# Optimization experiments

Hardware: AMD Instinct MI355X
Metric: run time of the kernel (lower is better)

Reference implementation:

```python
import jax, jax.numpy as jnp
import numpy as np

B = 1024          # batch of subject-object pairs
D_IN_HALF = 2048  # sbj/obj feature width; cat -> input_len = 4096
D_OUT = 1024      # output_len (embedding / label-vec width)
N_LABELS = 128    # number of relation labels in codebook


def setup_inputs() -> dict:
    key = jax.random.key(0)
    ks = jax.random.split(key, 7)
    s = 0.02  # small init scale for weights
    return {
        "sbj_vec": jax.random.normal(ks[0], (B, D_IN_HALF), jnp.float32),
        "obj_vec": jax.random.normal(ks[1], (B, D_IN_HALF), jnp.float32),
        "W1": jax.random.normal(ks[2], (2 * D_IN_HALF, D_OUT), jnp.float32) * s,
        "b1": jax.random.normal(ks[3], (D_OUT,), jnp.float32) * s,
        "W2": jax.random.normal(ks[4], (D_OUT, D_OUT), jnp.float32) * s,
        "b2": jax.random.normal(ks[5], (D_OUT,), jnp.float32) * s,
        "label_vecs": jax.random.normal(ks[6], (N_LABELS, D_OUT), jnp.float32),
    }


def reference(sbj_vec, obj_vec, W1, b1, W2, b2, label_vecs):
    # Sequential(ReLU, Dropout(eval=identity), Linear) applied twice.
    x = jnp.concatenate([sbj_vec, obj_vec], axis=1)          # [B, 2*D_IN_HALF]
    hidden = jax.nn.relu(x) @ W1 + b1                        # [B, D_OUT]
    emb = jax.nn.relu(hidden) @ W2 + b2                      # [B, D_OUT]
    # order_sim vs every label vector, fully batched (replaces per-sample loop):
    # sim[b, l] = -|| relu(label_vecs[l] - emb[b]) ||_2
    diff = jax.nn.relu(label_vecs[None, :, :] - emb[:, None, :])  # [B, L, D_OUT]
    scores = -jnp.sqrt(jnp.sum(diff * diff, axis=2))              # [B, L]
    return scores
```

## Files before the change

### kernel.cpp

```cpp
#include <hip/hip_runtime.h>
#include <math.h>

constexpr int Bn = 1024, DH = 2048, K1 = 4096, DO = 1024, NL = 128;
constexpr int MN = Bn * DO;

typedef __bf16 bf16x8 __attribute__((ext_vector_type(8)));
typedef short  s16x8  __attribute__((ext_vector_type(8)));
typedef float  f32x4  __attribute__((ext_vector_type(4)));

__device__ __forceinline__ unsigned short f2bf(float f) {
  union { float f; unsigned u; } v; v.f = f;
  unsigned r = v.u + 0x7FFFu + ((v.u >> 16) & 1u);
  return (unsigned short)(r >> 16);
}
__device__ __forceinline__ float bf2f(unsigned h) {
  union { unsigned u; float f; } v; v.u = h << 16; return v.f;
}

__global__ __launch_bounds__(256)
void prep(const float* __restrict__ sbj, const float* __restrict__ obj,
          const float* __restrict__ W1, const float* __restrict__ W2,
          unsigned short* __restrict__ Abf,
          unsigned short* __restrict__ W1t, unsigned short* __restrict__ W2t) {
  const int tid = threadIdx.x;
  if (blockIdx.x < 2048) {
    const int t = blockIdx.x * 256 + tid;
    const int m = t >> 9;
    const int k = (t & 511) << 3;
    const float* src = (k < DH) ? sbj + (size_t)m * DH + k
                                : obj + (size_t)m * DH + (k - DH);
    const float4 a = ((const float4*)src)[0];
    const float4 b = ((const float4*)src)[1];
    uint4 o;
    o.x = (unsigned)f2bf(fmaxf(a.x, 0.f)) | ((unsigned)f2bf(fmaxf(a.y, 0.f)) << 16);
    o.y = (unsigned)f2bf(fmaxf(a.z, 0.f)) | ((unsigned)f2bf(fmaxf(a.w, 0.f)) << 16);
    o.z = (unsigned)f2bf(fmaxf(b.x, 0.f)) | ((unsigned)f2bf(fmaxf(b.y, 0.f)) << 16);
    o.w = (unsigned)f2bf(fmaxf(b.z, 0.f)) | ((unsigned)f2bf(fmaxf(b.w, 0.f)) << 16);
    *(uint4*)&Abf[(size_t)m * K1 + k] = o;
    return;
  }
  __shared__ float tl[64][65];
  const int tb = blockIdx.x - 2048;
  int by = tb >> 4;
  const int c0 = (tb & 15) * 64;
  const float* in; unsigned short* out; int R;
  if (by < 64) { in = W1; out = W1t; R = K1; }
  else         { in = W2; out = W2t; R = DO; by -= 64; }
  const int r0 = by * 64;
  {
    const int rr = tid >> 4, cc = (tid & 15) * 4;
    #pragma unroll
    for (int i = 0; i < 4; ++i) {
      const float4 v = *(const float4*)&in[(size_t)(r0 + rr + i * 16) * DO + c0 + cc];
      tl[rr + i * 16][cc + 0] = v.x; tl[rr + i * 16][cc + 1] = v.y;
      tl[rr + i * 16][cc + 2] = v.z; tl[rr + i * 16][cc + 3] = v.w;
    }
  }
  __syncthreads();
  {
    const int r4 = (tid & 15) * 4;
    #pragma unroll
    for (int i = 0; i < 4; ++i) {
      const int cr = i * 16 + (tid >> 4);
      uint2 o;
      o.x = (unsigned)f2bf(tl[r4 + 0][cr]) | ((unsigned)f2bf(tl[r4 + 1][cr]) << 16);
      o.y = (unsigned)f2bf(tl[r4 + 2][cr]) | ((unsigned)f2bf(tl[r4 + 3][cr]) << 16);
      *(uint2*)&out[(size_t)(c0 + cr) * R + r0 + r4] = o;
    }
  }
}

template <int KSLICE>
__global__ __launch_bounds__(256, 2)
void mfma_gemm(const unsigned short* __restrict__ A,
               const unsigned short* __restrict__ Bt,
               unsigned short* __restrict__ P, int K) {
  __shared__ __align__(16) unsigned short smem[2][2 * 128 * 64];

  const int tid = threadIdx.x;
  const int w = tid >> 6, l = tid & 63;
  const int bid = blockIdx.x;
  const int z = bid & 7, t = bid >> 3;
  const int m0 = (t >> 3) * 128, n0 = (t & 7) * 128;
  const int kb = z * KSLICE;

  f32x4 acc[4][4] = {};

  constexpr int NIT = KSLICE / 64;

  auto stage = [&](int buf, int it) {
    const int k0 = kb + it * 64;
    unsigned short* LA = smem[buf];
    unsigned short* LB = smem[buf] + 128 * 64;
    #pragma unroll
    for (int i = 0; i < 4; ++i) {
      const int c = i * 256 + tid, row = c >> 3, kc = c & 7;
      const int kcg = kc ^ (row & 7);
      __builtin_amdgcn_global_load_lds(
          (const __attribute__((address_space(1))) unsigned int*)(A + (size_t)(m0 + row) * K + k0 + kcg * 8),
          (__attribute__((address_space(3))) unsigned int*)&LA[c * 8], 16, 0, 0);
    }
    #pragma unroll
    for (int i = 0; i < 4; ++i) {
      const int c = i * 256 + tid, row = c >> 3, kc = c & 7;
      const int kcg = kc ^ (row & 7);
      __builtin_amdgcn_global_load_lds(
          (const __attribute__((address_space(1))) unsigned int*)(Bt + (size_t)(n0 + row) * K + k0 + kcg * 8),
          (__attribute__((address_space(3))) unsigned int*)&LB[c * 8], 16, 0, 0);
    }
  };

  stage(0, 0);
  int cur = 0;
  for (int it = 0; it < NIT; ++it) {
    __syncthreads();
    if (it + 1 < NIT) stage(cur ^ 1, it + 1);

    const unsigned short* LA = smem[cur];
    const unsigned short* LB = smem[cur] + 128 * 64;
    #pragma unroll
    for (int s = 0; s < 2; ++s) {
      const int kcq = s * 4 + (l >> 4);
      bf16x8 af[4], bfr[4];
      #pragma unroll
      for (int i = 0; i < 4; ++i) {
        const int r = (w >> 1) * 64 + i * 16 + (l & 15);
        const int kca = kcq ^ (r & 7);
        af[i] = __builtin_bit_cast(bf16x8, *(const s16x8*)&LA[(r * 8 + kca) * 8]);
      }
      #pragma unroll
      for (int j = 0; j < 4; ++j) {
        const int rr = (w & 1) * 64 + j * 16 + (l & 15);
        const int kcb = kcq ^ (rr & 7);
        bfr[j] = __builtin_bit_cast(bf16x8, *(const s16x8*)&LB[(rr * 8 + kcb) * 8]);
      }
      #pragma unroll
      for (int i = 0; i < 4; ++i)
        #pragma unroll
        for (int j = 0; j < 4; ++j)
          acc[i][j] = __builtin_amdgcn_mfma_f32_16x16x32_bf16(af[i], bfr[j], acc[i][j], 0, 0, 0);
    }
    cur ^= 1;
  }

  unsigned short* Pz = P + (size_t)z * MN;
  #pragma unroll
  for (int i = 0; i < 4; ++i) {
    #pragma unroll
    for (int r = 0; r < 4; ++r) {
      const int m = m0 + (w >> 1) * 64 + i * 16 + (l >> 4) * 4 + r;
      #pragma unroll
      for (int j = 0; j < 4; ++j) {
        const int n = n0 + (w & 1) * 64 + j * 16 + (l & 15);
        Pz[(size_t)m * DO + n] = f2bf(acc[i][j][r]);
      }
    }
  }
}

__global__ __launch_bounds__(256)
void combine1(const unsigned short* __restrict__ P, const float* __restrict__ bias,
              unsigned short* __restrict__ out) {
  const int row = blockIdx.x, t = threadIdx.x;
  const size_t base = (size_t)row * DO + t * 4;
  float s0 = 0.f, s1 = 0.f, s2 = 0.f, s3 = 0.f;
  #pragma unroll
  for (int c = 0; c < 8; ++c) {
    const uint2 wv = *(const uint2*)&P[(size_t)c * MN + base];
    s0 += bf2f(wv.x & 0xFFFFu); s1 += bf2f(wv.x >> 16);
    s2 += bf2f(wv.y & 0xFFFFu); s3 += bf2f(wv.y >> 16);
  }
  const f32x4 bb = *(const f32x4*)&bias[t * 4];
  s0 = fmaxf(s0 + bb[0], 0.f); s1 = fmaxf(s1 + bb[1], 0.f);
  s2 = fmaxf(s2 + bb[2], 0.f); s3 = fmaxf(s3 + bb[3], 0.f);
  uint2 o;
  o.x = (unsigned)f2bf(s0) | ((unsigned)f2bf(s1) << 16);
  o.y = (unsigned)f2bf(s2) | ((unsigned)f2bf(s3) << 16);
  *(uint2*)&out[base] = o;
}

__global__ __launch_bounds__(256, 2)
void gemm2_full(const unsigned short* __restrict__ A,
                const unsigned short* __restrict__ Bt,
                const float* __restrict__ b2, float* __restrict__ E) {
  __shared__ __align__(16) unsigned short smem[2][2 * 64 * 128];

  const int tid = threadIdx.x;
  const int w = tid >> 6, l = tid & 63;
  const int bid = blockIdx.x;
  const int m0 = (bid >> 4) * 64, n0 = (bid & 15) * 64;

  f32x4 acc[4][4] = {};

  auto stage = [&](int buf, int it) {
    const int k0 = it * 128;
    unsigned short* LA = smem[buf];
    unsigned short* LB = smem[buf] + 64 * 128;
    #pragma unroll
    for (int i = 0; i < 4; ++i) {
      const int c = i * 256 + tid, m = c >> 4, kc = c & 15;
      const int kcg = (kc & 8) | ((kc & 7) ^ (m & 7));
      __builtin_amdgcn_global_load_lds(
          (const __attribute__((address_space(1))) unsigned int*)(A + (size_t)(m0 + m) * DO + k0 + kcg * 8),
          (__attribute__((address_space(3))) unsigned int*)&LA[c * 8], 16, 0, 0);
    }
    #pragma unroll
    for (int i = 0; i < 4; ++i) {
      const int c = i * 256 + tid, n = c >> 4, kc = c & 15;
      const int kcg = (kc & 8) | ((kc & 7) ^ (n & 7));
      __builtin_amdgcn_global_load_lds(
          (const __attribute__((address_space(1))) unsigned int*)(Bt + (size_t)(n0 + n) * DO + k0 + kcg * 8),
          (__attribute__((address_space(3))) unsigned int*)&LB[c * 8], 16, 0, 0);
    }
  };

  stage(0, 0);
  int cur = 0;
  for (int it = 0; it < 8; ++it) {
    __syncthreads();
    if (it + 1 < 8) stage(cur ^ 1, it + 1);

    const unsigned short* LA = smem[cur];
    const unsigned short* LB = smem[cur] + 64 * 128;
    const int kcq = w * 4 + (l >> 4);
    bf16x8 af[4], bfr[4];
    #pragma unroll
    for (int i = 0; i < 4; ++i) {
      const int r = i * 16 + (l & 15);
      const int kca = (kcq & 8) | ((kcq & 7) ^ (r & 7));
      af[i]  = __builtin_bit_cast(bf16x8, *(const s16x8*)&LA[(r * 16 + kca) * 8]);
      bfr[i] = __builtin_bit_cast(bf16x8, *(const s16x8*)&LB[(r * 16 + kca) * 8]);
    }
    #pragma unroll
    for (int i = 0; i < 4; ++i)
      #pragma unroll
      for (int j = 0; j < 4; ++j)
        acc[i][j] = __builtin_amdgcn_mfma_f32_16x16x32_bf16(af[i], bfr[j], acc[i][j], 0, 0, 0);
    cur ^= 1;
  }
  __syncthreads();

  float* red = (float*)smem;
  if (w >= 2) {
    #pragma unroll
    for (int i = 0; i < 4; ++i)
      #pragma unroll
      for (int j = 0; j < 4; ++j)
        *(f32x4*)&red[(w - 2) * 4096 + ((i * 4 + j) * 64 + l) * 4] = acc[i][j];
  }
  __syncthreads();
  if (w < 2) {
    #pragma unroll
    for (int i = 0; i < 4; ++i)
      #pragma unroll
      for (int j = 0; j < 4; ++j)
        acc[i][j] += *(const f32x4*)&red[w * 4096 + ((i * 4 + j) * 64 + l) * 4];
  }
  __syncthreads();
  if (w == 1) {
    #pragma unroll
    for (int i = 0; i < 2; ++i)
      #pragma unroll
      for (int j = 0; j < 4; ++j)
        *(f32x4*)&red[((i * 4 + j) * 64 + l) * 4] = acc[i][j];
  } else if (w == 0) {
    #pragma unroll
    for (int i = 0; i < 2; ++i)
      #pragma unroll
      for (int j = 0; j < 4; ++j)
        *(f32x4*)&red[2048 + ((i * 4 + j) * 64 + l) * 4] = acc[i + 2][j];
  }
  __syncthreads();
  if (w >= 2) return;

  if (w == 0) {
    #pragma unroll
    for (int i = 0; i < 2; ++i) {
      #pragma unroll
      for (int j = 0; j < 4; ++j)
        acc[i][j] += *(const f32x4*)&red[((i * 4 + j) * 64 + l) * 4];
      #pragma unroll
      for (int r = 0; r < 4; ++r) {
        const int m = m0 + i * 16 + (l >> 4) * 4 + r;
        #pragma unroll
        for (int j = 0; j < 4; ++j) {
          const int n = n0 + j * 16 + (l & 15);
          E[(size_t)m * DO + n] = acc[i][j][r] + b2[n];
        }
      }
    }
  } else {
    #pragma unroll
    for (int i = 0; i < 2; ++i) {
      #pragma unroll
      for (int j = 0; j < 4; ++j)
        acc[i + 2][j] += *(const f32x4*)&red[2048 + ((i * 4 + j) * 64 + l) * 4];
      #pragma unroll
      for (int r = 0; r < 4; ++r) {
        const int m = m0 + (i + 2) * 16 + (l >> 4) * 4 + r;
        #pragma unroll
        for (int j = 0; j < 4; ++j) {
          const int n = n0 + j * 16 + (l & 15);
          E[(size_t)m * DO + n] = acc[i + 2][j][r] + b2[n];
        }
      }
    }
  }
}

__global__ __launch_bounds__(256)
void score_partial(const float* __restrict__ E, const float* __restrict__ labels,
                   float* __restrict__ SP) {
  __shared__ float es[64][33];
  __shared__ float ls[64][132];
  const int tid = threadIdx.x;
  const int b0 = blockIdx.x * 32;

  const int tb = tid & 15;
  const int tl = tid >> 4;
  float acc[2][8] = {};

  #pragma unroll
  for (int ch = 0; ch < 2; ++ch) {
    const int d0 = blockIdx.y * 128 + ch * 64;
    if (ch) __syncthreads();

    #pragma unroll
    for (int i = 0; i < 2; ++i) {
      const int fi = tid + i * 256;
      const int b = fi >> 4, dq = fi & 15;
      const float4 v = *(const float4*)&E[(size_t)(b0 + b) * DO + d0 + dq * 4];
      es[dq * 4 + 0][b] = v.x; es[dq * 4 + 1][b] = v.y;
      es[dq * 4 + 2][b] = v.z; es[dq * 4 + 3][b] = v.w;
    }
    #pragma unroll
    for (int i = 0; i < 8; ++i) {
      const int fi = tid + i * 256;
      const int lr = fi >> 4, dq = fi & 15;
      const float4 v = *(const float4*)&labels[(size_t)lr * DO + d0 + dq * 4];
      ls[dq * 4 + 0][lr] = v.x; ls[dq * 4 + 1][lr] = v.y;
      ls[dq * 4 + 2][lr] = v.z; ls[dq * 4 + 3][lr] = v.w;
    }
    __syncthreads();

    for (int dd = 0; dd < 64; ++dd) {
      const float e0 = es[dd][tb * 2 + 0];
      const float e1 = es[dd][tb * 2 + 1];
      const float4 l0 = *(const float4*)&ls[dd][tl * 8];
      const float4 l1 = *(const float4*)&ls[dd][tl * 8 + 4];
      const float lv[8] = {l0.x, l0.y, l0.z, l0.w, l1.x, l1.y, l1.z, l1.w};
      #pragma unroll
      for (int j = 0; j < 8; ++j) {
        float t0 = fmaxf(lv[j] - e0, 0.f); acc[0][j] = fmaf(t0, t0, acc[0][j]);
        float t1 = fmaxf(lv[j] - e1, 0.f); acc[1][j] = fmaf(t1, t1, acc[1][j]);
      }
    }
  }

  float* SPz = SP + (size_t)blockIdx.y * (Bn * NL);
  #pragma unroll
  for (int i = 0; i < 2; ++i) {
    const size_t base = (size_t)(b0 + tb * 2 + i) * NL + tl * 8;
    float4 v0 = {acc[i][0], acc[i][1], acc[i][2], acc[i][3]};
    float4 v1 = {acc[i][4], acc[i][5], acc[i][6], acc[i][7]};
    *(float4*)&SPz[base]     = v0;
    *(float4*)&SPz[base + 4] = v1;
  }
}

__global__ __launch_bounds__(256)
void score_reduce(const float* __restrict__ SP, float* __restrict__ out) {
  const size_t i4 = (size_t)blockIdx.x * 256 + threadIdx.x;
  f32x4 s = ((const f32x4*)SP)[i4];
  #pragma unroll
  for (int c = 1; c < 8; ++c) s += ((const f32x4*)SP)[(size_t)c * 32768 + i4];
  f32x4 o = {-sqrtf(s[0]), -sqrtf(s[1]), -sqrtf(s[2]), -sqrtf(s[3])};
  ((f32x4*)out)[i4] = o;
}

extern "C" void kernel_launch(void* const* d_in, const int* in_sizes, int n_in,
                              void* d_out, int out_size, void* d_ws, size_t ws_size,
                              hipStream_t stream) {
  const float* sbj  = (const float*)d_in[0];
  const float* obj  = (const float*)d_in[1];
  const float* W1   = (const float*)d_in[2];
  const float* b1   = (const float*)d_in[3];
  const float* W2   = (const float*)d_in[4];
  const float* b2   = (const float*)d_in[5];
  const float* labs = (const float*)d_in[6];
  float* scores = (float*)d_out;
  char* ws = (char*)d_ws;

  unsigned short* Abf = (unsigned short*)(ws);
  unsigned short* W1t = (unsigned short*)(ws + (8ull << 20));
  unsigned short* W2t = (unsigned short*)(ws + (16ull << 20));
  unsigned short* H   = (unsigned short*)(ws + (18ull << 20));
  float* E  = (float*)(ws + (20ull << 20));
  unsigned short* P = (unsigned short*)(ws + (24ull << 20));
  float* SP = (float*)(ws + (40ull << 20));

  dim3 blk(256);
  prep<<<dim3(2048 + 1280), blk, 0, stream>>>(sbj, obj, W1, W2, Abf, W1t, W2t);

  mfma_gemm<512><<<dim3(512), blk, 0, stream>>>(Abf, W1t, P, K1);
  combine1<<<dim3(Bn), blk, 0, stream>>>(P, b1, H);
  gemm2_full<<<dim3(256), blk, 0, stream>>>(H, W2t, b2, E);
  score_partial<<<dim3(32, 8), blk, 0, stream>>>(E, labs, SP);
  score_reduce<<<dim3(128), blk, 0, stream>>>(SP, scores);
}
```

Before: 133.6 us.

## Fuse activation ReLU and bf16 conversion into GEMM1 A-tile loading

Removes the prep pass that wrote a bf16 copy of the concatenated ReLU'd activations. GEMM1 now loads fp32 sbj/obj tiles into registers, applies ReLU, converts to bf16 and writes them to swizzled LDS, with the global load overlapped with the MFMA loop. This saves a full write and re-read of the 8 MB bf16 activation buffer, at the cost of more register pressure and ALU work inside the GEMM. combine1 is also widened to 8 elements per thread with half as many blocks.

Result: no change. 136.2 us (+2.0%).

```diff
diff --git a/kernel.cpp b/kernel.cpp
--- a/kernel.cpp
+++ b/kernel.cpp
@@ -18,29 +18,11 @@
 }
 
 __global__ __launch_bounds__(256)
-void prep(const float* __restrict__ sbj, const float* __restrict__ obj,
-          const float* __restrict__ W1, const float* __restrict__ W2,
-          unsigned short* __restrict__ Abf,
+void prep(const float* __restrict__ W1, const float* __restrict__ W2,
           unsigned short* __restrict__ W1t, unsigned short* __restrict__ W2t) {
   const int tid = threadIdx.x;
-  if (blockIdx.x < 2048) {
-    const int t = blockIdx.x * 256 + tid;
-    const int m = t >> 9;
-    const int k = (t & 511) << 3;
-    const float* src = (k < DH) ? sbj + (size_t)m * DH + k
-                                : obj + (size_t)m * DH + (k - DH);
-    const float4 a = ((const float4*)src)[0];
-    const float4 b = ((const float4*)src)[1];
-    uint4 o;
-    o.x = (unsigned)f2bf(fmaxf(a.x, 0.f)) | ((unsigned)f2bf(fmaxf(a.y, 0.f)) << 16);
-    o.y = (unsigned)f2bf(fmaxf(a.z, 0.f)) | ((unsigned)f2bf(fmaxf(a.w, 0.f)) << 16);
-    o.z = (unsigned)f2bf(fmaxf(b.x, 0.f)) | ((unsigned)f2bf(fmaxf(b.y, 0.f)) << 16);
-    o.w = (unsigned)f2bf(fmaxf(b.z, 0.f)) | ((unsigned)f2bf(fmaxf(b.w, 0.f)) << 16);
-    *(uint4*)&Abf[(size_t)m * K1 + k] = o;
-    return;
-  }
   __shared__ float tl[64][65];
-  const int tb = blockIdx.x - 2048;
+  const int tb = blockIdx.x;
   int by = tb >> 4;
   const int c0 = (tb & 15) * 64;
   const float* in; unsigned short* out; int R;
@@ -72,9 +54,9 @@
 
 template <int KSLICE>
 __global__ __launch_bounds__(256, 2)
-void mfma_gemm(const unsigned short* __restrict__ A,
+void mfma_gemm(const float* __restrict__ sbj, const float* __restrict__ obj,
                const unsigned short* __restrict__ Bt,
-               unsigned short* __restrict__ P, int K) {
+               unsigned short* __restrict__ P) {
   __shared__ __align__(16) unsigned short smem[2][2 * 128 * 64];
 
   const int tid = threadIdx.x;
@@ -84,37 +66,62 @@
   const int m0 = (t >> 3) * 128, n0 = (t & 7) * 128;
   const int kb = z * KSLICE;
 
+  const float* __restrict__ Asrc = (z < 4) ? sbj : obj;
+  const int cb = kb - ((z < 4) ? 0 : DH);
+
   f32x4 acc[4][4] = {};
+  float4 areg[4][2];
 
   constexpr int NIT = KSLICE / 64;
 
-  auto stage = [&](int buf, int it) {
+  auto loadA = [&](int it) {
+    const int col0 = cb + it * 64;
+    #pragma unroll
+    for (int i = 0; i < 4; ++i) {
+      const int cc = i * 256 + tid, row = cc >> 3, kc = cc & 7;
+      const float* p = Asrc + (size_t)(m0 + row) * DH + col0 + kc * 8;
+      areg[i][0] = ((const float4*)p)[0];
+      areg[i][1] = ((const float4*)p)[1];
+    }
+  };
+  auto writeA = [&](int buf) {
+    unsigned short* LA = smem[buf];
+    #pragma unroll
+    for (int i = 0; i < 4; ++i) {
+      const int cc = i * 256 + tid, row = cc >> 3, kc = cc & 7;
+      const int kcg = kc ^ (row & 7);
+      const float4 a = areg[i][0], b = areg[i][1];
+      bf16x8 h;
+      h[0] = (__bf16)fmaxf(a.x, 0.f); h[1] = (__bf16)fmaxf(a.y, 0.f);
+      h[2] = (__bf16)fmaxf(a.z, 0.f); h[3] = (__bf16)fmaxf(a.w, 0.f);
+      h[4] = (__bf16)fmaxf(b.x, 0.f); h[5] = (__bf16)fmaxf(b.y, 0.f);
+      h[6] = (__bf16)fmaxf(b.z, 0.f); h[7] = (__bf16)fmaxf(b.w, 0.f);
+      *(bf16x8*)&LA[(row * 8 + kcg) * 8] = h;
+    }
+  };
+  auto stageB = [&](int buf, int it) {
     const int k0 = kb + it * 64;
-    unsigned short* LA = smem[buf];
     unsigned short* LB = smem[buf] + 128 * 64;
     #pragma unroll
     for (int i = 0; i < 4; ++i) {
       const int c = i * 256 + tid, row = c >> 3, kc = c & 7;
       const int kcg = kc ^ (row & 7);
       __builtin_amdgcn_global_load_lds(
-          (const __attribute__((address_space(1))) unsigned int*)(A + (size_t)(m0 + row) * K + k0 + kcg * 8),
-          (__attribute__((address_space(3))) unsigned int*)&LA[c * 8], 16, 0, 0);
-    }
-    #pragma unroll
-    for (int i = 0; i < 4; ++i) {
-      const int c = i * 256 + tid, row = c >> 3, kc = c & 7;
-      const int kcg = kc ^ (row & 7);
-      __builtin_amdgcn_global_load_lds(
-          (const __attribute__((address_space(1))) unsigned int*)(Bt + (size_t)(n0 + row) * K + k0 + kcg * 8),
+          (const __attribute__((address_space(1))) unsigned int*)(Bt + (size_t)(n0 + row) * K1 + k0 + kcg * 8),
           (__attribute__((address_space(3))) unsigned int*)&LB[c * 8], 16, 0, 0);
     }
   };
 
-  stage(0, 0);
+  loadA(0);
+  stageB(0, 0);
+  writeA(0);
   int cur = 0;
   for (int it = 0; it < NIT; ++it) {
     __syncthreads();
-    if (it + 1 < NIT) stage(cur ^ 1, it + 1);
+    if (it + 1 < NIT) {
+      loadA(it + 1);
+      stageB(cur ^ 1, it + 1);
+    }
 
     const unsigned short* LA = smem[cur];
     const unsigned short* LB = smem[cur] + 128 * 64;
@@ -140,6 +147,7 @@
         for (int j = 0; j < 4; ++j)
           acc[i][j] = __builtin_amdgcn_mfma_f32_16x16x32_bf16(af[i], bfr[j], acc[i][j], 0, 0, 0);
     }
+    if (it + 1 < NIT) writeA(cur ^ 1);
     cur ^= 1;
   }
 
@@ -161,22 +169,31 @@
 __global__ __launch_bounds__(256)
 void combine1(const unsigned short* __restrict__ P, const float* __restrict__ bias,
               unsigned short* __restrict__ out) {
-  const int row = blockIdx.x, t = threadIdx.x;
-  const size_t base = (size_t)row * DO + t * 4;
-  float s0 = 0.f, s1 = 0.f, s2 = 0.f, s3 = 0.f;
+  const int t = threadIdx.x;
+  const int row = blockIdx.x * 2 + (t >> 7);
+  const int col = (t & 127) * 8;
+  const size_t base = (size_t)row * DO + col;
+  float s[8] = {};
   #pragma unroll
   for (int c = 0; c < 8; ++c) {
-    const uint2 wv = *(const uint2*)&P[(size_t)c * MN + base];
-    s0 += bf2f(wv.x & 0xFFFFu); s1 += bf2f(wv.x >> 16);
-    s2 += bf2f(wv.y & 0xFFFFu); s3 += bf2f(wv.y >> 16);
-  }
-  const f32x4 bb = *(const f32x4*)&bias[t * 4];
-  s0 = fmaxf(s0 + bb[0], 0.f); s1 = fmaxf(s1 + bb[1], 0.f);
-  s2 = fmaxf(s2 + bb[2], 0.f); s3 = fmaxf(s3 + bb[3], 0.f);
-  uint2 o;
-  o.x = (unsigned)f2bf(s0) | ((unsigned)f2bf(s1) << 16);
-  o.y = (unsigned)f2bf(s2) | ((unsigned)f2bf(s3) << 16);
-  *(uint2*)&out[base] = o;
+    const uint4 wv = *(const uint4*)&P[(size_t)c * MN + base];
+    s[0] += bf2f(wv.x & 0xFFFFu); s[1] += bf2f(wv.x >> 16);
+    s[2] += bf2f(wv.y & 0xFFFFu); s[3] += bf2f(wv.y >> 16);
+    s[4] += bf2f(wv.z & 0xFFFFu); s[5] += bf2f(wv.z >> 16);
+    s[6] += bf2f(wv.w & 0xFFFFu); s[7] += bf2f(wv.w >> 16);
+  }
+  const f32x4 b0 = *(const f32x4*)&bias[col];
+  const f32x4 b1v = *(const f32x4*)&bias[col + 4];
+  #pragma unroll
+  for (int i = 0; i < 4; ++i) s[i] = fmaxf(s[i] + b0[i], 0.f);
+  #pragma unroll
+  for (int i = 0; i < 4; ++i) s[4 + i] = fmaxf(s[4 + i] + b1v[i], 0.f);
+  uint4 o;
+  o.x = (unsigned)f2bf(s[0]) | ((unsigned)f2bf(s[1]) << 16);
+  o.y = (unsigned)f2bf(s[2]) | ((unsigned)f2bf(s[3]) << 16);
+  o.z = (unsigned)f2bf(s[4]) | ((unsigned)f2bf(s[5]) << 16);
+  o.w = (unsigned)f2bf(s[6]) | ((unsigned)f2bf(s[7]) << 16);
+  *(uint4*)&out[base] = o;
 }
 
 __global__ __launch_bounds__(256, 2)
@@ -391,7 +408,6 @@
   float* scores = (float*)d_out;
   char* ws = (char*)d_ws;
 
-  unsigned short* Abf = (unsigned short*)(ws);
   unsigned short* W1t = (unsigned short*)(ws + (8ull << 20));
   unsigned short* W2t = (unsigned short*)(ws + (16ull << 20));
   unsigned short* H   = (unsigned short*)(ws + (18ull << 20));
@@ -400,10 +416,10 @@
   float* SP = (float*)(ws + (40ull << 20));
 
   dim3 blk(256);
-  prep<<<dim3(2048 + 1280), blk, 0, stream>>>(sbj, obj, W1, W2, Abf, W1t, W2t);
-
-  mfma_gemm<512><<<dim3(512), blk, 0, stream>>>(Abf, W1t, P, K1);
-  combine1<<<dim3(Bn), blk, 0, stream>>>(P, b1, H);
+  prep<<<dim3(1280), blk, 0, stream>>>(W1, W2, W1t, W2t);
+
+  mfma_gemm<512><<<dim3(512), blk, 0, stream>>>(sbj, obj, W1t, P);
+  combine1<<<dim3(512), blk, 0, stream>>>(P, b1, H);
   gemm2_full<<<dim3(256), blk, 0, stream>>>(H, W2t, b2, E);
   score_partial<<<dim3(32, 8), blk, 0, stream>>>(E, labs, SP);
   score_reduce<<<dim3(128), blk, 0, stream>>>(SP, scores);
```

## Split-K second GEMM in two and fold partial sum and bias into scoring

Applied to the files above, without the earlier changes.

The second GEMM now splits K into two halves across 512 blocks instead of 256, writing two fp32 partial outputs. The scoring kernel sums the two partials and adds b2 while loading its tile, so no separate reduction kernel is needed. The combine kernel is also widened to 8 elements per thread with 16-byte loads and half the blocks. The aim is better CU occupancy for the small GEMM at the cost of an extra 4 MB of partial writes and reads.

New measurement: 135.8 us. Within noise of the previous version (+1.7%).

```diff
diff --git a/kernel.cpp b/kernel.cpp
--- a/kernel.cpp
+++ b/kernel.cpp
@@ -161,39 +161,50 @@
 __global__ __launch_bounds__(256)
 void combine1(const unsigned short* __restrict__ P, const float* __restrict__ bias,
               unsigned short* __restrict__ out) {
-  const int row = blockIdx.x, t = threadIdx.x;
-  const size_t base = (size_t)row * DO + t * 4;
-  float s0 = 0.f, s1 = 0.f, s2 = 0.f, s3 = 0.f;
+  const int t = threadIdx.x;
+  const int row = blockIdx.x * 2 + (t >> 7);
+  const int col = (t & 127) * 8;
+  const size_t base = (size_t)row * DO + col;
+  float s[8] = {};
   #pragma unroll
   for (int c = 0; c < 8; ++c) {
-    const uint2 wv = *(const uint2*)&P[(size_t)c * MN + base];
-    s0 += bf2f(wv.x & 0xFFFFu); s1 += bf2f(wv.x >> 16);
-    s2 += bf2f(wv.y & 0xFFFFu); s3 += bf2f(wv.y >> 16);
-  }
-  const f32x4 bb = *(const f32x4*)&bias[t * 4];
-  s0 = fmaxf(s0 + bb[0], 0.f); s1 = fmaxf(s1 + bb[1], 0.f);
-  s2 = fmaxf(s2 + bb[2], 0.f); s3 = fmaxf(s3 + bb[3], 0.f);
-  uint2 o;
-  o.x = (unsigned)f2bf(s0) | ((unsigned)f2bf(s1) << 16);
-  o.y = (unsigned)f2bf(s2) | ((unsigned)f2bf(s3) << 16);
-  *(uint2*)&out[base] = o;
+    const uint4 wv = *(const uint4*)&P[(size_t)c * MN + base];
+    s[0] += bf2f(wv.x & 0xFFFFu); s[1] += bf2f(wv.x >> 16);
+    s[2] += bf2f(wv.y & 0xFFFFu); s[3] += bf2f(wv.y >> 16);
+    s[4] += bf2f(wv.z & 0xFFFFu); s[5] += bf2f(wv.z >> 16);
+    s[6] += bf2f(wv.w & 0xFFFFu); s[7] += bf2f(wv.w >> 16);
+  }
+  const f32x4 b0 = *(const f32x4*)&bias[col];
+  const f32x4 b1v = *(const f32x4*)&bias[col + 4];
+  #pragma unroll
+  for (int i = 0; i < 4; ++i) s[i] = fmaxf(s[i] + b0[i], 0.f);
+  #pragma unroll
+  for (int i = 0; i < 4; ++i) s[4 + i] = fmaxf(s[4 + i] + b1v[i], 0.f);
+  uint4 o;
+  o.x = (unsigned)f2bf(s[0]) | ((unsigned)f2bf(s[1]) << 16);
+  o.y = (unsigned)f2bf(s[2]) | ((unsigned)f2bf(s[3]) << 16);
+  o.z = (unsigned)f2bf(s[4]) | ((unsigned)f2bf(s[5]) << 16);
+  o.w = (unsigned)f2bf(s[6]) | ((unsigned)f2bf(s[7]) << 16);
+  *(uint4*)&out[base] = o;
 }
 
 __global__ __launch_bounds__(256, 2)
-void gemm2_full(const unsigned short* __restrict__ A,
-                const unsigned short* __restrict__ Bt,
-                const float* __restrict__ b2, float* __restrict__ E) {
+void gemm2_sk(const unsigned short* __restrict__ A,
+              const unsigned short* __restrict__ Bt,
+              float* __restrict__ E2) {
   __shared__ __align__(16) unsigned short smem[2][2 * 64 * 128];
 
   const int tid = threadIdx.x;
   const int w = tid >> 6, l = tid & 63;
   const int bid = blockIdx.x;
-  const int m0 = (bid >> 4) * 64, n0 = (bid & 15) * 64;
+  const int z2 = bid & 1, t = bid >> 1;
+  const int m0 = (t >> 4) * 64, n0 = (t & 15) * 64;
+  const int kb = z2 * 512;
 
   f32x4 acc[4][4] = {};
 
   auto stage = [&](int buf, int it) {
-    const int k0 = it * 128;
+    const int k0 = kb + it * 128;
     unsigned short* LA = smem[buf];
     unsigned short* LB = smem[buf] + 64 * 128;
     #pragma unroll
@@ -216,9 +227,9 @@
 
   stage(0, 0);
   int cur = 0;
-  for (int it = 0; it < 8; ++it) {
+  for (int it = 0; it < 4; ++it) {
     __syncthreads();
-    if (it + 1 < 8) stage(cur ^ 1, it + 1);
+    if (it + 1 < 4) stage(cur ^ 1, it + 1);
 
     const unsigned short* LA = smem[cur];
     const unsigned short* LB = smem[cur] + 64 * 128;
@@ -273,6 +284,7 @@
   __syncthreads();
   if (w >= 2) return;
 
+  float* Ez = E2 + (size_t)z2 * MN;
   if (w == 0) {
     #pragma unroll
     for (int i = 0; i < 2; ++i) {
@@ -285,7 +297,7 @@
         #pragma unroll
         for (int j = 0; j < 4; ++j) {
           const int n = n0 + j * 16 + (l & 15);
-          E[(size_t)m * DO + n] = acc[i][j][r] + b2[n];
+          Ez[(size_t)m * DO + n] = acc[i][j][r];
         }
       }
     }
@@ -301,7 +313,7 @@
         #pragma unroll
         for (int j = 0; j < 4; ++j) {
           const int n = n0 + j * 16 + (l & 15);
-          E[(size_t)m * DO + n] = acc[i + 2][j][r] + b2[n];
+          Ez[(size_t)m * DO + n] = acc[i + 2][j][r];
         }
       }
     }
@@ -309,8 +321,8 @@
 }
 
 __global__ __launch_bounds__(256)
-void score_partial(const float* __restrict__ E, const float* __restrict__ labels,
-                   float* __restrict__ SP) {
+void score_partial(const float* __restrict__ E2, const float* __restrict__ b2,
+                   const float* __restrict__ labels, float* __restrict__ SP) {
   __shared__ float es[64][33];
   __shared__ float ls[64][132];
   const int tid = threadIdx.x;
@@ -329,9 +341,14 @@
     for (int i = 0; i < 2; ++i) {
       const int fi = tid + i * 256;
       const int b = fi >> 4, dq = fi & 15;
-      const float4 v = *(const float4*)&E[(size_t)(b0 + b) * DO + d0 + dq * 4];
-      es[dq * 4 + 0][b] = v.x; es[dq * 4 + 1][b] = v.y;
-      es[dq * 4 + 2][b] = v.z; es[dq * 4 + 3][b] = v.w;
+      const size_t eoff = (size_t)(b0 + b) * DO + d0 + dq * 4;
+      const float4 v0 = *(const float4*)&E2[eoff];
+      const float4 v1 = *(const float4*)&E2[(size_t)MN + eoff];
+      const float4 bb = *(const float4*)&b2[d0 + dq * 4];
+      es[dq * 4 + 0][b] = v0.x + v1.x + bb.x;
+      es[dq * 4 + 1][b] = v0.y + v1.y + bb.y;
+      es[dq * 4 + 2][b] = v0.z + v1.z + bb.z;
+      es[dq * 4 + 3][b] = v0.w + v1.w + bb.w;
     }
     #pragma unroll
     for (int i = 0; i < 8; ++i) {
@@ -395,16 +412,16 @@
   unsigned short* W1t = (unsigned short*)(ws + (8ull << 20));
   unsigned short* W2t = (unsigned short*)(ws + (16ull << 20));
   unsigned short* H   = (unsigned short*)(ws + (18ull << 20));
-  float* E  = (float*)(ws + (20ull << 20));
-  unsigned short* P = (unsigned short*)(ws + (24ull << 20));
-  float* SP = (float*)(ws + (40ull << 20));
+  unsigned short* P   = (unsigned short*)(ws + (20ull << 20));
+  float* E2 = (float*)(ws + (36ull << 20));
+  float* SP = (float*)(ws + (44ull << 20));
 
   dim3 blk(256);
   prep<<<dim3(2048 + 1280), blk, 0, stream>>>(sbj, obj, W1, W2, Abf, W1t, W2t);
 
   mfma_gemm<512><<<dim3(512), blk, 0, stream>>>(Abf, W1t, P, K1);
-  combine1<<<dim3(Bn), blk, 0, stream>>>(P, b1, H);
-  gemm2_full<<<dim3(256), blk, 0, stream>>>(H, W2t, b2, E);
-  score_partial<<<dim3(32, 8), blk, 0, stream>>>(E, labs, SP);
+  combine1<<<dim3(512), blk, 0, stream>>>(P, b1, H);
+  gemm2_sk<<<dim3(512), blk, 0, stream>>>(H, W2t, E2);
+  score_partial<<<dim3(32, 8), blk, 0, stream>>>(E2, b2, labs, SP);
   score_reduce<<<dim3(128), blk, 0, stream>>>(SP, scores);
 }
```

## Fuse score reduction into score_partial via last-block atomic counter; widen combine1 loads

Applied to the files above, without the earlier changes.

Drops the separate score_reduce launch. Each score_partial block now publishes its partial sums with release stores and bumps a per-row-group counter, and the last of the 8 blocks in that group reduces the partials and writes -sqrt. The counters are zeroed inside prep. combine1 also moves to 128-bit loads and stores, handling two rows per block with half as many blocks. In exchange, the partial stores become scalar atomic stores and the final reduction runs in only 32 tail blocks, which may serialize.

Result: slower. 371.4 us (+178.0%).

```diff
diff --git a/kernel.cpp b/kernel.cpp
--- a/kernel.cpp
+++ b/kernel.cpp
@@ -3,6 +3,7 @@
 
 constexpr int Bn = 1024, DH = 2048, K1 = 4096, DO = 1024, NL = 128;
 constexpr int MN = Bn * DO;
+constexpr int SPS = Bn * NL;
 
 typedef __bf16 bf16x8 __attribute__((ext_vector_type(8)));
 typedef short  s16x8  __attribute__((ext_vector_type(8)));
@@ -21,7 +22,8 @@
 void prep(const float* __restrict__ sbj, const float* __restrict__ obj,
           const float* __restrict__ W1, const float* __restrict__ W2,
           unsigned short* __restrict__ Abf,
-          unsigned short* __restrict__ W1t, unsigned short* __restrict__ W2t) {
+          unsigned short* __restrict__ W1t, unsigned short* __restrict__ W2t,
+          int* __restrict__ cnt) {
   const int tid = threadIdx.x;
   if (blockIdx.x < 2048) {
     const int t = blockIdx.x * 256 + tid;
@@ -41,6 +43,7 @@
   }
   __shared__ float tl[64][65];
   const int tb = blockIdx.x - 2048;
+  if (tb == 0 && tid < 32) cnt[tid] = 0;
   int by = tb >> 4;
   const int c0 = (tb & 15) * 64;
   const float* in; unsigned short* out; int R;
@@ -161,22 +164,31 @@
 __global__ __launch_bounds__(256)
 void combine1(const unsigned short* __restrict__ P, const float* __restrict__ bias,
               unsigned short* __restrict__ out) {
-  const int row = blockIdx.x, t = threadIdx.x;
-  const size_t base = (size_t)row * DO + t * 4;
-  float s0 = 0.f, s1 = 0.f, s2 = 0.f, s3 = 0.f;
+  const int t = threadIdx.x;
+  const int row = blockIdx.x * 2 + (t >> 7);
+  const int col = (t & 127) * 8;
+  const size_t base = (size_t)row * DO + col;
+  float s[8] = {};
   #pragma unroll
   for (int c = 0; c < 8; ++c) {
-    const uint2 wv = *(const uint2*)&P[(size_t)c * MN + base];
-    s0 += bf2f(wv.x & 0xFFFFu); s1 += bf2f(wv.x >> 16);
-    s2 += bf2f(wv.y & 0xFFFFu); s3 += bf2f(wv.y >> 16);
-  }
-  const f32x4 bb = *(const f32x4*)&bias[t * 4];
-  s0 = fmaxf(s0 + bb[0], 0.f); s1 = fmaxf(s1 + bb[1], 0.f);
-  s2 = fmaxf(s2 + bb[2], 0.f); s3 = fmaxf(s3 + bb[3], 0.f);
-  uint2 o;
-  o.x = (unsigned)f2bf(s0) | ((unsigned)f2bf(s1) << 16);
-  o.y = (unsigned)f2bf(s2) | ((unsigned)f2bf(s3) << 16);
-  *(uint2*)&out[base] = o;
+    const uint4 wv = *(const uint4*)&P[(size_t)c * MN + base];
+    s[0] += bf2f(wv.x & 0xFFFFu); s[1] += bf2f(wv.x >> 16);
+    s[2] += bf2f(wv.y & 0xFFFFu); s[3] += bf2f(wv.y >> 16);
+    s[4] += bf2f(wv.z & 0xFFFFu); s[5] += bf2f(wv.z >> 16);
+    s[6] += bf2f(wv.w & 0xFFFFu); s[7] += bf2f(wv.w >> 16);
+  }
+  const f32x4 b0 = *(const f32x4*)&bias[col];
+  const f32x4 b1v = *(const f32x4*)&bias[col + 4];
+  #pragma unroll
+  for (int i = 0; i < 4; ++i) s[i] = fmaxf(s[i] + b0[i], 0.f);
+  #pragma unroll
+  for (int i = 0; i < 4; ++i) s[4 + i] = fmaxf(s[4 + i] + b1v[i], 0.f);
+  uint4 o;
+  o.x = (unsigned)f2bf(s[0]) | ((unsigned)f2bf(s[1]) << 16);
+  o.y = (unsigned)f2bf(s[2]) | ((unsigned)f2bf(s[3]) << 16);
+  o.z = (unsigned)f2bf(s[4]) | ((unsigned)f2bf(s[5]) << 16);
+  o.w = (unsigned)f2bf(s[6]) | ((unsigned)f2bf(s[7]) << 16);
+  *(uint4*)&out[base] = o;
 }
 
 __global__ __launch_bounds__(256, 2)
@@ -310,9 +322,11 @@
 
 __global__ __launch_bounds__(256)
 void score_partial(const float* __restrict__ E, const float* __restrict__ labels,
-                   float* __restrict__ SP) {
+                   float* __restrict__ SP, int* __restrict__ cnt,
+                   float* __restrict__ out) {
   __shared__ float es[64][33];
   __shared__ float ls[64][132];
+  __shared__ int last;
   const int tid = threadIdx.x;
   const int b0 = blockIdx.x * 32;
 
@@ -357,25 +371,34 @@
     }
   }
 
-  float* SPz = SP + (size_t)blockIdx.y * (Bn * NL);
+  float* SPz = SP + (size_t)blockIdx.y * SPS;
   #pragma unroll
   for (int i = 0; i < 2; ++i) {
     const size_t base = (size_t)(b0 + tb * 2 + i) * NL + tl * 8;
-    float4 v0 = {acc[i][0], acc[i][1], acc[i][2], acc[i][3]};
-    float4 v1 = {acc[i][4], acc[i][5], acc[i][6], acc[i][7]};
-    *(float4*)&SPz[base]     = v0;
-    *(float4*)&SPz[base + 4] = v1;
-  }
-}
-
-__global__ __launch_bounds__(256)
-void score_reduce(const float* __restrict__ SP, float* __restrict__ out) {
-  const size_t i4 = (size_t)blockIdx.x * 256 + threadIdx.x;
-  f32x4 s = ((const f32x4*)SP)[i4];
-  #pragma unroll
-  for (int c = 1; c < 8; ++c) s += ((const f32x4*)SP)[(size_t)c * 32768 + i4];
-  f32x4 o = {-sqrtf(s[0]), -sqrtf(s[1]), -sqrtf(s[2]), -sqrtf(s[3])};
-  ((f32x4*)out)[i4] = o;
+    #pragma unroll
+    for (int j = 0; j < 8; ++j)
+      __hip_atomic_store(&SPz[base + j], acc[i][j],
+                         __ATOMIC_RELEASE, __HIP_MEMORY_SCOPE_AGENT);
+  }
+  __syncthreads();
+  if (tid == 0)
+    last = __hip_atomic_fetch_add(&cnt[blockIdx.x], 1,
+                                  __ATOMIC_ACQ_REL, __HIP_MEMORY_SCOPE_AGENT);
+  __syncthreads();
+  if (last != 7) return;
+
+  #pragma unroll
+  for (int q = 0; q < 16; ++q) {
+    const int idx = tid * 16 + q;
+    const int b = idx >> 7, l = idx & 127;
+    const size_t off = (size_t)(b0 + b) * NL + l;
+    float s = 0.f;
+    #pragma unroll
+    for (int c = 0; c < 8; ++c)
+      s += __hip_atomic_load(&SP[(size_t)c * SPS + off],
+                             __ATOMIC_ACQUIRE, __HIP_MEMORY_SCOPE_AGENT);
+    out[off] = -sqrtf(s);
+  }
 }
 
 extern "C" void kernel_launch(void* const* d_in, const int* in_sizes, int n_in,
@@ -398,13 +421,13 @@
   float* E  = (float*)(ws + (20ull << 20));
   unsigned short* P = (unsigned short*)(ws + (24ull << 20));
   float* SP = (float*)(ws + (40ull << 20));
+  int*   cnt = (int*)(ws + (44ull << 20));
 
   dim3 blk(256);
-  prep<<<dim3(2048 + 1280), blk, 0, stream>>>(sbj, obj, W1, W2, Abf, W1t, W2t);
+  prep<<<dim3(2048 + 1280), blk, 0, stream>>>(sbj, obj, W1, W2, Abf, W1t, W2t, cnt);
 
   mfma_gemm<512><<<dim3(512), blk, 0, stream>>>(Abf, W1t, P, K1);
-  combine1<<<dim3(Bn), blk, 0, stream>>>(P, b1, H);
+  combine1<<<dim3(512), blk, 0, stream>>>(P, b1, H);
   gemm2_full<<<dim3(256), blk, 0, stream>>>(H, W2t, b2, E);
-  score_partial<<<dim3(32, 8), blk, 0, stream>>>(E, labs, SP);
-  score_reduce<<<dim3(128), blk, 0, stream>>>(SP, scores);
-}
+  score_partial<<<dim3(32, 8), blk, 0, stream>>>(E, labs, SP, cnt, scores);
+}
```
